# Kernel tuning notes

Hardware: AMD Instinct MI355X
Metric: run time of the kernel (lower is better)

The kernel has to match this reference:

```python
import jax, jax.numpy as jnp
import numpy as np
from jax import lax

B, NC, H, W = 8, 128, 64, 64
INP = 2 * NC            # 256 input_ch
UP = INP * 4            # 1024 upscaled_ch (r1=4)
MD = UP // 8            # 128 mamba_dim (r2=8)
IC = UP // 2            # 512 ghost init_channels (ratio=2)
DIN = 2 * MD            # 256 d_inner (expand=2)
DST = 1                 # d_state
DCONV = 4               # d_conv
DTR = 8                 # dt_rank = ceil(MD/16)
EPS = 1e-5

def _n(k, shape, fan):
    return jax.random.normal(k, shape, jnp.float32) / np.sqrt(fan)

def setup_inputs() -> dict:
    ks = jax.random.split(jax.random.key(0), 16)
    d = {}
    d['FT1'] = jax.random.normal(ks[0], (B, NC, H, W), jnp.float32)
    d['FT2'] = jax.random.normal(ks[1], (B, NC, H, W), jnp.float32)
    # GhostModule(inp=256, oup=1024): 1x1 primary + 3x3 depthwise cheap op
    d['g_primary_w'] = _n(ks[2], (IC, INP, 1, 1), INP)
    d['g_bn1_g'] = jnp.ones((IC,)); d['g_bn1_b'] = jnp.zeros((IC,))
    d['g_bn1_m'] = jnp.zeros((IC,)); d['g_bn1_v'] = jnp.ones((IC,))
    d['g_cheap_w'] = _n(ks[3], (IC, 1, 3, 3), 9)
    d['g_bn2_g'] = jnp.ones((IC,)); d['g_bn2_b'] = jnp.zeros((IC,))
    d['g_bn2_m'] = jnp.zeros((IC,)); d['g_bn2_v'] = jnp.ones((IC,))
    # SELayer(channel=1024, reduction=16), Linear bias=False
    d['se_w1'] = _n(ks[4], (UP // 16, UP), UP)
    d['se_w2'] = _n(ks[5], (UP, UP // 16), UP // 16)
    # 1x1 conv 1024->128 + BN
    d['proj_w'] = _n(ks[6], (MD, UP, 1, 1), UP)
    d['bn3_g'] = jnp.ones((MD,)); d['bn3_b'] = jnp.zeros((MD,))
    d['bn3_m'] = jnp.zeros((MD,)); d['bn3_v'] = jnp.ones((MD,))
    # Mamba(d_model=128, d_state=1, d_conv=4, expand=2)
    d['in_proj_w'] = _n(ks[7], (2 * DIN, MD), MD)
    d['conv1d_w'] = _n(ks[8], (DIN, 1, DCONV), DCONV)
    d['conv1d_b'] = jnp.zeros((DIN,))
    d['x_proj_w'] = _n(ks[9], (DTR + 2 * DST, DIN), DIN)
    d['dt_proj_w'] = _n(ks[10], (DIN, DTR), DTR)
    d['dt_proj_b'] = jnp.log(jnp.expm1(jnp.full((DIN,), 0.01)))  # softplus^-1(0.01)
    d['A_log'] = jnp.zeros((DIN, DST))  # A = -exp(0) = -1 (d_state=1 init)
    d['Dp'] = jnp.ones((DIN,))
    d['out_proj_w'] = _n(ks[11], (MD, DIN), DIN)
    # GatedResidual linear_pi: Linear(2*MD, MD) with bias
    d['pi_w'] = _n(ks[12], (MD, 2 * MD), 2 * MD)
    d['pi_b'] = jnp.zeros((MD,))
    # final 1x1 conv 128->128, no bias
    d['final_w'] = _n(ks[13], (NC, MD, 1, 1), MD)
    return d

def _bn(x, g, b, m, v):
    return (x - m[:, None, None]) * (g[:, None, None] / jnp.sqrt(v[:, None, None] + EPS)) + b[:, None, None]

def _conv2d(x, w, groups=1, pad=0):
    return lax.conv_general_dilated(x, w, (1, 1), [(pad, pad), (pad, pad)],
        dimension_numbers=('NCHW', 'OIHW', 'NCHW'), feature_group_count=groups)

def _mamba(x, in_proj_w, conv1d_w, conv1d_b, x_proj_w, dt_proj_w, dt_proj_b, A_log, Dp, out_proj_w):
    # x: (N, L, MD)
    N, L, _ = x.shape
    xz = x @ in_proj_w.T                    # (N,L,2*DIN)
    xs, z = jnp.split(xz, 2, axis=-1)
    # causal depthwise conv1d (pytorch pads d_conv-1 both sides then truncates to L)
    xc = jnp.moveaxis(xs, 1, 2)             # (N,DIN,L)
    xc = lax.conv_general_dilated(xc, conv1d_w, (1,), [(DCONV - 1, 0)],
        dimension_numbers=('NCH', 'OIH', 'NCH'), feature_group_count=DIN) + conv1d_b[:, None]
    u = jax.nn.silu(jnp.moveaxis(xc, 1, 2))  # (N,L,DIN)
    dbl = u @ x_proj_w.T                     # (N,L,DTR+2*DST)
    dt, Bm, Cm = dbl[..., :DTR], dbl[..., DTR:DTR + DST], dbl[..., DTR + DST:]
    dt = jax.nn.softplus(dt @ dt_proj_w.T + dt_proj_b)  # (N,L,DIN)
    A = -jnp.exp(A_log)                      # (DIN,DST)

    def step(h, inp):
        u_, dt_, B_, C_ = inp                # (N,DIN),(N,DIN),(N,DST),(N,DST)
        h = h * jnp.exp(dt_[:, :, None] * A) + dt_[:, :, None] * B_[:, None, :] * u_[:, :, None]
        return h, jnp.sum(h * C_[:, None, :], axis=-1)

    h0 = jnp.zeros((N, DIN, DST), x.dtype)
    _, y_t = lax.scan(step, h0, (jnp.moveaxis(u, 0, 1), jnp.moveaxis(dt, 0, 1),
                                 jnp.moveaxis(Bm, 0, 1), jnp.moveaxis(Cm, 0, 1)))
    y = jnp.moveaxis(y_t, 0, 1) + u * Dp
    y = y * jax.nn.silu(z)
    return y @ out_proj_w.T                  # (N,L,MD)

def reference(FT1, FT2, g_primary_w, g_bn1_g, g_bn1_b, g_bn1_m, g_bn1_v,
              g_cheap_w, g_bn2_g, g_bn2_b, g_bn2_m, g_bn2_v, se_w1, se_w2,
              proj_w, bn3_g, bn3_b, bn3_m, bn3_v, in_proj_w, conv1d_w, conv1d_b,
              x_proj_w, dt_proj_w, dt_proj_b, A_log, Dp, out_proj_w,
              pi_w, pi_b, final_w):
    Fcat = jnp.concatenate([FT1, FT2], axis=1)                       # (B,256,H,W)
    # GhostModule
    x1 = jax.nn.relu(_bn(_conv2d(Fcat, g_primary_w), g_bn1_g, g_bn1_b, g_bn1_m, g_bn1_v))
    x2 = jax.nn.relu(_bn(_conv2d(x1, g_cheap_w, groups=IC, pad=1), g_bn2_g, g_bn2_b, g_bn2_m, g_bn2_v))
    g = jnp.concatenate([x1, x2], axis=1)[:, :UP]                    # (B,1024,H,W)
    # SELayer
    s = jnp.mean(g, axis=(2, 3))
    s = jax.nn.sigmoid(jax.nn.relu(s @ se_w1.T) @ se_w2.T)
    g = g * s[:, :, None, None]
    Fp = _bn(_conv2d(g, proj_w), bn3_g, bn3_b, bn3_m, bn3_v)         # (B,MD,H,W)
    # four-way scan
    X_lr = jnp.transpose(Fp, (0, 2, 3, 1)).reshape(B, H * W, MD)
    X_rl = jnp.transpose(Fp[:, :, :, ::-1], (0, 2, 3, 1)).reshape(B, H * W, MD)
    X_ud = jnp.transpose(Fp, (0, 3, 2, 1)).reshape(B, H * W, MD)
    X_du = jnp.transpose(Fp[:, :, ::-1, :], (0, 3, 2, 1)).reshape(B, H * W, MD)
    X4 = jnp.stack([X_lr, X_rl, X_ud, X_du]).reshape(4 * B, H * W, MD)
    # shared Mamba block over all 4 directions in one batched call
    Y4 = _mamba(X4, in_proj_w, conv1d_w, conv1d_b, x_proj_w, dt_proj_w, dt_proj_b, A_log, Dp, out_proj_w)
    # gated residual
    pi = jax.nn.sigmoid(jnp.concatenate([X4, Y4], axis=-1) @ pi_w.T + pi_b)
    Yg = Y4 * pi + X4 * (1.0 - pi)
    # four-way inverse scan (sum, then row-major reshape as in source)
    y_sum = jnp.sum(Yg.reshape(4, B, H * W, MD), axis=0)
    f_scan = jnp.transpose(y_sum.reshape(B, H, W, MD), (0, 3, 1, 2))
    return _conv2d(f_scan + Fp, final_w)                             # (B,NC,H,W)
```

## Files before the change

kernel.cpp:

```cpp
#include <hip/hip_runtime.h>
#include <hip/hip_bf16.h>

#define DEV static __device__ __forceinline__

#define PIX 4096
#define SEQL 4096
#define BEPS 1e-5f

DEV float b2f(unsigned short u){ unsigned int i=((unsigned int)u)<<16; float f; __builtin_memcpy(&f,&i,4); return f; }
DEV unsigned short f2b(float f){ __hip_bfloat16 h=__float2bfloat16(f); unsigned short s; __builtin_memcpy(&s,&h,2); return s; }
DEV short f2bs(float f){ return (short)f2b(f); }
DEV void unp2(unsigned int w, float&a, float&b){ unsigned int lo=w<<16, hi=w&0xffff0000u; __builtin_memcpy(&a,&lo,4); __builtin_memcpy(&b,&hi,4); }
DEV unsigned int pk2(float a,float b){ return (unsigned int)f2b(a)|((unsigned int)f2b(b)<<16); }
DEV float sigm(float x){ return 1.f/(1.f+__expf(-x)); }
DEV float silu_(float x){ return x*sigm(x); }
DEV float softplus_(float x){ return (x>20.f)?x:log1pf(__expf(x)); }

using short8 = __attribute__((ext_vector_type(8))) short;
using f32x4  = __attribute__((ext_vector_type(4))) float;
#define MFMA16 __builtin_amdgcn_mfma_f32_16x16x32_bf16


#define MF_PRE() \
  const int tid=threadIdx.x; \
  const int lane=tid&63, wid=tid>>6; \
  const int wm=wid&1, wn=wid>>1; \
  const int fr=lane&15, fg=lane>>4; \
  const int srow=tid>>2, sch=tid&3; \
  const int tk=tid&63, tmb=(tid>>6)*16;

#define STAGE_A_TOK_BF(PTR) { \
  const unsigned short* ap_=(PTR); \
  uint4 q0_=*(const uint4*)ap_, q1_=*(const uint4*)(ap_+8); \
  int base_=srow*72+((sch^(srow&3))*16); \
  *(uint4*)&sA[base_]=q0_; *(uint4*)&sA[base_+8]=q1_; }

#define STAGE_A_SUM_BF(P1,P2) { \
  const unsigned short* p1_=(P1); const unsigned short* p2_=(P2); \
  unsigned short h1[16],h2[16]; \
  *(uint4*)&h1[0]=*(const uint4*)p1_; *(uint4*)&h1[8]=*(const uint4*)(p1_+8); \
  *(uint4*)&h2[0]=*(const uint4*)p2_; *(uint4*)&h2[8]=*(const uint4*)(p2_+8); \
  union { short h[16]; uint4 q[2]; } tmpa; \
  _Pragma("unroll") for(int j=0;j<16;++j) tmpa.h[j]=f2bs(b2f(h1[j])+b2f(h2[j])); \
  int base_=srow*72+((sch^(srow&3))*16); \
  *(uint4*)&sA[base_]=tmpa.q[0]; *(uint4*)&sA[base_+8]=tmpa.q[1]; }

#define STAGE_A_TR_F32(EXPR16) { \
  float tv[16]; \
  _Pragma("unroll") for(int j=0;j<16;++j) tv[j]=(EXPR16); \
  _Pragma("unroll") for(int j=0;j<16;++j){ int m_=tmb+j; \
    sA[m_*72+(((tk>>4)^(m_&3))<<4)+(tk&15)]=f2bs(tv[j]); } }

#define STAGE_A_TR_BF16(PTR) { \
  const unsigned short* ap_=(PTR); \
  unsigned short hv[16]; \
  *(uint4*)&hv[0]=*(const uint4*)ap_; *(uint4*)&hv[8]=*(const uint4*)(ap_+8); \
  _Pragma("unroll") for(int j=0;j<16;++j){ int m_=tmb+j; \
    sA[m_*72+(((tk>>4)^(m_&3))<<4)+(tk&15)]=(short)hv[j]; } }

#define STAGE_W_BF(PTR,LDK) { \
  const unsigned short* wp_=(PTR)+(size_t)(n0+srow)*(LDK)+k0+sch*16; \
  uint4 q0_=*(const uint4*)wp_, q1_=*(const uint4*)(wp_+8); \
  int sw_=((sch^(srow&3))*16); \
  *(uint4*)&sW[srow*72+sw_]=q0_; *(uint4*)&sW[srow*72+sw_+8]=q1_; }

#define MF_STEP() \
  _Pragma("unroll") \
  for(int kk=0;kk<64;kk+=32){ \
    short8 af[2],bfv[2]; const int kq_=kk+fg*8; \
    _Pragma("unroll") for(int i=0;i<2;++i){ int ml=wm*32+i*16+fr; \
      af[i]=*(const short8*)&sA[ml*72+(((kq_>>4)^(ml&3))<<4)+(kq_&15)]; } \
    _Pragma("unroll") for(int jn=0;jn<2;++jn){ int nl=wn*32+jn*16+fr; \
      bfv[jn]=*(const short8*)&sW[nl*72+(((kq_>>4)^(nl&3))<<4)+(kq_&15)]; } \
    _Pragma("unroll") for(int i=0;i<2;++i) \
      _Pragma("unroll") for(int jn=0;jn<2;++jn) \
        acc[i][jn]=MFMA16(af[i],bfv[jn],acc[i][jn],0,0,0); }

__global__ __launch_bounds__(256) void kWb(const float* __restrict__ g,const float* __restrict__ ip,
  const float* __restrict__ op,const float* __restrict__ pw,const float* __restrict__ f,
  unsigned short* __restrict__ gb,unsigned short* __restrict__ ib,unsigned short* __restrict__ ob,
  unsigned short* __restrict__ pb,unsigned short* __restrict__ fb)
{
  int x=blockIdx.x*256+threadIdx.x;
  if(x<131072) gb[x]=f2b(g[x]);
  if(x<65536)  ib[x]=f2b(ip[x]);
  if(x<32768){ ob[x]=f2b(op[x]); pb[x]=f2b(pw[x]); }
  if(x<16384)  fb[x]=f2b(f[x]);
}

__global__ __launch_bounds__(256) void kWc(const float* __restrict__ dtw,const float* __restrict__ xpw,
  unsigned short* __restrict__ Wcb)
{
  int c=blockIdx.x, k=threadIdx.x;
  float a=0.f;
  #pragma unroll
  for(int i=0;i<8;++i) a+=dtw[c*8+i]*xpw[i*256+k];
  Wcb[c*256+k]=f2b(a);
}

__global__ __launch_bounds__(256) void kWse(const float* __restrict__ prw,const float* __restrict__ sse,
  unsigned short* __restrict__ Wsb)
{
  int idx=blockIdx.x*256+threadIdx.x;
  int b=idx>>17, r=idx&131071, oc=r>>10, c=r&1023;
  Wsb[idx]=f2b(prw[(size_t)oc*1024+c]*sse[b*1024+c]);
}

__global__ __launch_bounds__(256) void k1m(const float* __restrict__ FT1,const float* __restrict__ FT2,
  const unsigned short* __restrict__ Wpb,const float* __restrict__ gg,const float* __restrict__ gb,
  const float* __restrict__ gm,const float* __restrict__ gv,unsigned short* __restrict__ x1)
{
  MF_PRE();
  __shared__ __align__(16) short sA[64*72];
  __shared__ __align__(16) short sW[64*72];
  const int m0=blockIdx.x*64, n0=blockIdx.y*64, b=blockIdx.z;
  f32x4 acc[2][2]={};
  for(int k0=0;k0<256;k0+=64){
    { int c=k0+tk;
      const float* s_=(c<128)? FT1+((size_t)b*128+c)*PIX : FT2+((size_t)b*128+c-128)*PIX;
      const float* ap=s_+m0+tmb;
      STAGE_A_TR_F32(ap[j]); }
    STAGE_W_BF(Wpb,256);
    __syncthreads();
    MF_STEP();
    __syncthreads();
  }
  #pragma unroll
  for(int jn=0;jn<2;++jn){ int oc=n0+wn*32+jn*16+fr;
    float ks=gg[oc]*rsqrtf(gv[oc]+BEPS), kb=gb[oc]-gm[oc]*ks;
    #pragma unroll
    for(int i=0;i<2;++i){ int mb=m0+wm*32+i*16+fg*4;
      float v0=fmaxf(acc[i][jn][0]*ks+kb,0.f), v1=fmaxf(acc[i][jn][1]*ks+kb,0.f);
      float v2=fmaxf(acc[i][jn][2]*ks+kb,0.f), v3=fmaxf(acc[i][jn][3]*ks+kb,0.f);
      uint2 pk; pk.x=pk2(v0,v1); pk.y=pk2(v2,v3);
      *(uint2*)&x1[((size_t)b*512+oc)*PIX+mb]=pk; } }
}

__global__ __launch_bounds__(256) void k2(const unsigned short* __restrict__ x1,const float* __restrict__ cw,
  const float* __restrict__ gg,const float* __restrict__ gb,const float* __restrict__ gm,
  const float* __restrict__ gv,unsigned short* __restrict__ x2)
{
  int gid=blockIdx.x*256+threadIdx.x;
  int wq=gid&15, h=(gid>>4)&63, bc=gid>>10;
  int c=bc&511;
  const unsigned short* src=x1+(size_t)bc*PIX;
  float wv[9];
  #pragma unroll
  for(int i=0;i<9;++i) wv[i]=cw[c*9+i];
  float ks=gg[c]*rsqrtf(gv[c]+BEPS), kb=gb[c]-gm[c]*ks;
  int wb=wq*4;
  float o[4]={};
  #pragma unroll
  for(int dh=0;dh<3;++dh){ int hh=h+dh-1; if(hh<0||hh>63) continue;
    const unsigned short* row=src+hh*64;
    float rv[6];
    #pragma unroll
    for(int j=0;j<6;++j){ int wc=wb-1+j; rv[j]=(wc>=0&&wc<64)?b2f(row[wc]):0.f; }
    #pragma unroll
    for(int dw=0;dw<3;++dw){ float wgt=wv[dh*3+dw];
      #pragma unroll
      for(int i=0;i<4;++i) o[i]+=rv[i+dw]*wgt; } }
  float v0=fmaxf(o[0]*ks+kb,0.f), v1=fmaxf(o[1]*ks+kb,0.f);
  float v2=fmaxf(o[2]*ks+kb,0.f), v3=fmaxf(o[3]*ks+kb,0.f);
  uint2 pk; pk.x=pk2(v0,v1); pk.y=pk2(v2,v3);
  *(uint2*)&x2[(size_t)bc*PIX+h*64+wb]=pk;
}

__global__ __launch_bounds__(256) void k3(const unsigned short* __restrict__ x1,
  const unsigned short* __restrict__ x2,float* __restrict__ sr)
{
  int bc=blockIdx.x; int cg=bc&1023, b=bc>>10;
  const unsigned short* src=(cg<512)? x1+((size_t)b*512+cg)*PIX : x2+((size_t)b*512+cg-512)*PIX;
  float s=0;
  for(int i=threadIdx.x;i<512;i+=256){
    uint4 v=((const uint4*)src)[i];
    float a0,a1; unp2(v.x,a0,a1); s+=a0+a1;
    unp2(v.y,a0,a1); s+=a0+a1;
    unp2(v.z,a0,a1); s+=a0+a1;
    unp2(v.w,a0,a1); s+=a0+a1;
  }
  #pragma unroll
  for(int off=32;off;off>>=1) s+=__shfl_down(s,off);
  __shared__ float red[4];
  if((threadIdx.x&63)==0) red[threadIdx.x>>6]=s;
  __syncthreads();
  if(threadIdx.x==0) sr[bc]=(red[0]+red[1]+red[2]+red[3])*(1.f/4096.f);
}

__global__ __launch_bounds__(256) void k4(const float* __restrict__ sr,const float* __restrict__ w1,
  const float* __restrict__ w2,float* __restrict__ sOut)
{
  int b=blockIdx.x;
  __shared__ float ls[1024];
  __shared__ float pm[4][64];
  __shared__ float mid[64];
  for(int i=threadIdx.x;i<1024;i+=256) ls[i]=sr[b*1024+i];
  __syncthreads();
  int k=threadIdx.x&63, part=threadIdx.x>>6;
  float p=0;
  for(int c=part*256;c<part*256+256;++c) p+=ls[c]*w1[k*1024+c];
  pm[part][k]=p;
  __syncthreads();
  if(threadIdx.x<64) mid[threadIdx.x]=fmaxf(pm[0][threadIdx.x]+pm[1][threadIdx.x]+pm[2][threadIdx.x]+pm[3][threadIdx.x],0.f);
  __syncthreads();
  for(int j=threadIdx.x;j<1024;j+=256){
    float a=0;
    for(int kk=0;kk<64;++kk) a+=mid[kk]*w2[j*64+kk];
    sOut[b*1024+j]=sigm(a);
  }
}

__global__ __launch_bounds__(256) void k5m(const unsigned short* __restrict__ x1,
  const unsigned short* __restrict__ x2,const unsigned short* __restrict__ Wsb,
  const float* __restrict__ g3,const float* __restrict__ b3,const float* __restrict__ m3,
  const float* __restrict__ v3,unsigned short* __restrict__ Fp,unsigned short* __restrict__ FpT)
{
  MF_PRE();
  __shared__ __align__(16) short sA[64*72];
  __shared__ __align__(16) short sW[64*72];
  const int m0=blockIdx.x*64, n0=blockIdx.y*64, b=blockIdx.z;
  const unsigned short* Wb=Wsb+(size_t)b*131072;
  f32x4 acc[2][2]={};
  for(int k0=0;k0<1024;k0+=64){
    { int c=k0+tk;
      const unsigned short* s_=(c<512)? x1+((size_t)b*512+c)*PIX : x2+((size_t)b*512+c-512)*PIX;
      STAGE_A_TR_BF16(s_+m0+tmb); }
    STAGE_W_BF(Wb,1024);
    __syncthreads();
    MF_STEP();
    __syncthreads();
  }
  #pragma unroll
  for(int jn=0;jn<2;++jn){ int oc=n0+wn*32+jn*16+fr;
    float ks=g3[oc]*rsqrtf(v3[oc]+BEPS), kb=b3[oc]-m3[oc]*ks;
    #pragma unroll
    for(int i=0;i<2;++i){ int mb=m0+wm*32+i*16+fg*4;
      #pragma unroll
      for(int p=0;p<4;++p){ int pp=mb+p; unsigned short val=f2b(acc[i][jn][p]*ks+kb);
        Fp[((size_t)b*PIX+pp)*128+oc]=val;
        int q=((pp&63)<<6)|(pp>>6);
        FpT[((size_t)b*PIX+q)*128+oc]=val; } } }
}

__global__ __launch_bounds__(256) void k6am(const unsigned short* __restrict__ Fp,
  const unsigned short* __restrict__ FpT,const unsigned short* __restrict__ Winb,
  unsigned short* __restrict__ xsT,unsigned short* __restrict__ zT)
{
  MF_PRE();
  __shared__ __align__(16) short sA[64*72];
  __shared__ __align__(16) short sW[64*72];
  const int m0=blockIdx.x*64, n0=blockIdx.y*64, n=blockIdx.z;
  const int d=n>>3, b=n&7;
  const unsigned short* src=((d<2)?Fp:FpT)+(size_t)b*PIX*128;
  const int rev=(d&1)?63:0;
  f32x4 acc[2][2]={};
  for(int k0=0;k0<128;k0+=64){
    { int t=m0+srow; int tm=(t&~63)|((t&63)^rev);
      STAGE_A_TOK_BF(src+(size_t)tm*128+k0+sch*16); }
    STAGE_W_BF(Winb,128);
    __syncthreads();
    MF_STEP();
    __syncthreads();
  }
  #pragma unroll
  for(int jn=0;jn<2;++jn){ int r=n0+wn*32+jn*16+fr;
    unsigned short* dst; int row; bool dosilu;
    if(r<256){ dst=xsT; row=r; dosilu=false; } else { dst=zT; row=r-256; dosilu=true; }
    #pragma unroll
    for(int i=0;i<2;++i){ int mb=m0+wm*32+i*16+fg*4;
      #pragma unroll
      for(int p=0;p<4;++p){ float v=acc[i][jn][p]; if(dosilu) v=silu_(v);
        dst[((size_t)n*SEQL+mb+p)*256+row]=f2b(v); } } }
}

__global__ __launch_bounds__(256) void k6b(const unsigned short* __restrict__ xsT,
  const float* __restrict__ cw,const float* __restrict__ cb,unsigned short* __restrict__ uT)
{
  int gid=blockIdx.x*256+threadIdx.x;
  int cb8=gid&31, tb=(gid>>5)&511, n=gid>>14;
  int c0=cb8*8, t0=tb*8;
  const unsigned short* base=xsT+(size_t)n*SEQL*256+c0;
  float w0[8],w1[8],w2[8],w3[8],bb[8];
  #pragma unroll
  for(int j=0;j<8;++j){ float4 wv=*(const float4*)&cw[(c0+j)*4];
    w0[j]=wv.x; w1[j]=wv.y; w2[j]=wv.z; w3[j]=wv.w; bb[j]=cb[c0+j]; }
  float ra[8],rb[8],rc[8],rd[8];
  #pragma unroll
  for(int j=0;j<8;++j){ ra[j]=0.f; rb[j]=0.f; rc[j]=0.f; }
  if(t0>=3){
    uint4 v;
    v=*(const uint4*)(base+(size_t)(t0-3)*256); unp2(v.x,ra[0],ra[1]);unp2(v.y,ra[2],ra[3]);unp2(v.z,ra[4],ra[5]);unp2(v.w,ra[6],ra[7]);
    v=*(const uint4*)(base+(size_t)(t0-2)*256); unp2(v.x,rb[0],rb[1]);unp2(v.y,rb[2],rb[3]);unp2(v.z,rb[4],rb[5]);unp2(v.w,rb[6],rb[7]);
    v=*(const uint4*)(base+(size_t)(t0-1)*256); unp2(v.x,rc[0],rc[1]);unp2(v.y,rc[2],rc[3]);unp2(v.z,rc[4],rc[5]);unp2(v.w,rc[6],rc[7]);
  }
  unsigned short* ob=uT+(size_t)n*SEQL*256+c0;
  for(int j=0;j<8;++j){
    uint4 v=*(const uint4*)(base+(size_t)(t0+j)*256);
    unp2(v.x,rd[0],rd[1]);unp2(v.y,rd[2],rd[3]);unp2(v.z,rd[4],rd[5]);unp2(v.w,rd[6],rd[7]);
    float o[8];
    #pragma unroll
    for(int q=0;q<8;++q){
      o[q]=silu_(ra[q]*w0[q]+rb[q]*w1[q]+rc[q]*w2[q]+rd[q]*w3[q]+bb[q]);
      ra[q]=rb[q]; rb[q]=rc[q]; rc[q]=rd[q];
    }
    uint4 ov; ov.x=pk2(o[0],o[1]); ov.y=pk2(o[2],o[3]); ov.z=pk2(o[4],o[5]); ov.w=pk2(o[6],o[7]);
    *(uint4*)(ob+(size_t)(t0+j)*256)=ov;
  }
}

__global__ __launch_bounds__(256) void k6cm(const unsigned short* __restrict__ uT,
  const unsigned short* __restrict__ Wcb,const float* __restrict__ dtb,
  unsigned short* __restrict__ dtT)
{
  MF_PRE();
  __shared__ __align__(16) short sA[64*72];
  __shared__ __align__(16) short sW[64*72];
  const int m0=blockIdx.x*64, n0=blockIdx.y*64, n=blockIdx.z;
  const unsigned short* ubase=uT+(size_t)n*SEQL*256;
  f32x4 acc[2][2]={};
  for(int k0=0;k0<256;k0+=64){
    STAGE_A_TOK_BF(ubase+(size_t)(m0+srow)*256+k0+sch*16);
    STAGE_W_BF(Wcb,256);
    __syncthreads();
    MF_STEP();
    __syncthreads();
  }
  #pragma unroll
  for(int jn=0;jn<2;++jn){ int oc=n0+wn*32+jn*16+fr;
    float bias=dtb[oc];
    #pragma unroll
    for(int i=0;i<2;++i){ int mb=m0+wm*32+i*16+fg*4;
      #pragma unroll
      for(int p=0;p<4;++p)
        dtT[((size_t)n*SEQL+mb+p)*256+oc]=f2b(softplus_(acc[i][jn][p]+bias)); } }
}

__global__ __launch_bounds__(256) void k6bc(const unsigned short* __restrict__ uT,
  const float* __restrict__ xpw,float* __restrict__ Bc,float* __restrict__ Cc)
{
  int inst=blockIdx.x*4+(threadIdx.x>>6);
  int ln=threadIdx.x&63;
  int n=inst>>12, t=inst&4095;
  const unsigned short* up=uT+((size_t)n*SEQL+t)*256+ln*4;
  uint2 uu=*(const uint2*)up;
  float u0,u1,u2,u3; unp2(uu.x,u0,u1); unp2(uu.y,u2,u3);
  float4 w8=*(const float4*)&xpw[8*256+ln*4];
  float4 w9=*(const float4*)&xpw[9*256+ln*4];
  float sb=u0*w8.x+u1*w8.y+u2*w8.z+u3*w8.w;
  float sc=u0*w9.x+u1*w9.y+u2*w9.z+u3*w9.w;
  #pragma unroll
  for(int off=32;off;off>>=1){ sb+=__shfl_xor(sb,off); sc+=__shfl_xor(sc,off); }
  if(ln==0){ Bc[(size_t)n*SEQL+t]=sb; Cc[(size_t)n*SEQL+t]=sc; }
}

__global__ __launch_bounds__(256) void k7p1(const unsigned short* __restrict__ uT,
  const unsigned short* __restrict__ dtT,const float* __restrict__ Bc,
  const float* __restrict__ A_log,float* __restrict__ Pq)
{
  int g=blockIdx.x*256+threadIdx.x;
  int cq=g&63, ch=(g>>6)&31, n=g>>11;
  int c0=cq*4;
  float A0=-__expf(A_log[c0]),A1=-__expf(A_log[c0+1]),A2=-__expf(A_log[c0+2]),A3=-__expf(A_log[c0+3]);
  size_t tbase=((size_t)n*SEQL+ch*128)*256+c0;
  const float* bp=Bc+(size_t)n*SEQL+ch*128;
  float P0=1,P1=1,P2=1,P3=1,q0=0,q1=0,q2=0,q3=0;
  for(int t=0;t<128;++t){
    uint2 uu=*(const uint2*)&uT[tbase+(size_t)t*256];
    uint2 dd=*(const uint2*)&dtT[tbase+(size_t)t*256];
    float u0,u1,u2,u3,d0,d1,d2,d3;
    unp2(uu.x,u0,u1); unp2(uu.y,u2,u3);
    unp2(dd.x,d0,d1); unp2(dd.y,d2,d3);
    float bv=bp[t];
    float e0=__expf(d0*A0),e1=__expf(d1*A1),e2=__expf(d2*A2),e3=__expf(d3*A3);
    q0=q0*e0+d0*bv*u0; q1=q1*e1+d1*bv*u1; q2=q2*e2+d2*bv*u2; q3=q3*e3+d3*bv*u3;
    P0*=e0; P1*=e1; P2*=e2; P3*=e3;
  }
  size_t o=(((size_t)n*256+c0)*32+ch)*2;
  Pq[o]=P0; Pq[o+1]=q0; Pq[o+64]=P1; Pq[o+65]=q1;
  Pq[o+128]=P2; Pq[o+129]=q2; Pq[o+192]=P3; Pq[o+193]=q3;
}

__global__ __launch_bounds__(256) void k7mid(const float* __restrict__ Pq,float* __restrict__ h0)
{
  int nc=blockIdx.x*256+threadIdx.x;
  float h=0.f;
  for(int ch=0;ch<32;++ch){
    h0[(size_t)nc*32+ch]=h;
    h=h*Pq[((size_t)nc*32+ch)*2]+Pq[((size_t)nc*32+ch)*2+1];
  }
}

__global__ __launch_bounds__(256) void k7p2(unsigned short* __restrict__ uT,
  const unsigned short* __restrict__ dtT,const unsigned short* __restrict__ zT,
  const float* __restrict__ Bc,const float* __restrict__ Cc,
  const float* __restrict__ A_log,const float* __restrict__ Dp,
  const float* __restrict__ h0)
{
  int g=blockIdx.x*256+threadIdx.x;
  int cq=g&63, ch=(g>>6)&31, n=g>>11;
  int c0=cq*4;
  float A0=-__expf(A_log[c0]),A1=-__expf(A_log[c0+1]),A2=-__expf(A_log[c0+2]),A3=-__expf(A_log[c0+3]);
  float D0=Dp[c0],D1=Dp[c0+1],D2=Dp[c0+2],D3=Dp[c0+3];
  size_t tbase=((size_t)n*SEQL+ch*128)*256+c0;
  const float* bp=Bc+(size_t)n*SEQL+ch*128;
  const float* cp=Cc+(size_t)n*SEQL+ch*128;
  size_t hb=((size_t)n*256+c0)*32+ch;
  float h0v=h0[hb],h1v=h0[hb+32],h2v=h0[hb+64],h3v=h0[hb+96];
  for(int t=0;t<128;++t){
    uint2 uu=*(const uint2*)&uT[tbase+(size_t)t*256];
    uint2 dd=*(const uint2*)&dtT[tbase+(size_t)t*256];
    uint2 zz=*(const uint2*)&zT[tbase+(size_t)t*256];
    float u0,u1,u2,u3,d0,d1,d2,d3,z0,z1,z2,z3;
    unp2(uu.x,u0,u1); unp2(uu.y,u2,u3);
    unp2(dd.x,d0,d1); unp2(dd.y,d2,d3);
    unp2(zz.x,z0,z1); unp2(zz.y,z2,z3);
    float bv=bp[t], cv=cp[t];
    float e0=__expf(d0*A0),e1=__expf(d1*A1),e2=__expf(d2*A2),e3=__expf(d3*A3);
    h0v=h0v*e0+d0*bv*u0; h1v=h1v*e1+d1*bv*u1; h2v=h2v*e2+d2*bv*u2; h3v=h3v*e3+d3*bv*u3;
    float y0=(h0v*cv+u0*D0)*z0, y1=(h1v*cv+u1*D1)*z1;
    float y2=(h2v*cv+u2*D2)*z2, y3=(h3v*cv+u3*D3)*z3;
    uint2 oo; oo.x=pk2(y0,y1); oo.y=pk2(y2,y3);
    *(uint2*)&uT[tbase+(size_t)t*256]=oo;
  }
}

__global__ __launch_bounds__(256) void k8am(const unsigned short* __restrict__ yT,
  const unsigned short* __restrict__ Woutb,unsigned short* __restrict__ Y4)
{
  MF_PRE();
  __shared__ __align__(16) short sA[64*72];
  __shared__ __align__(16) short sW[64*72];
  const int m0=blockIdx.x*64, n0=blockIdx.y*64, n=blockIdx.z;
  const unsigned short* ybase=yT+(size_t)n*SEQL*256;
  f32x4 acc[2][2]={};
  for(int k0=0;k0<256;k0+=64){
    STAGE_A_TOK_BF(ybase+(size_t)(m0+srow)*256+k0+sch*16);
    STAGE_W_BF(Woutb,256);
    __syncthreads();
    MF_STEP();
    __syncthreads();
  }
  #pragma unroll
  for(int jn=0;jn<2;++jn){ int oc=n0+wn*32+jn*16+fr;
    #pragma unroll
    for(int i=0;i<2;++i){ int mb=m0+wm*32+i*16+fg*4;
      #pragma unroll
      for(int p=0;p<4;++p)
        Y4[((size_t)n*SEQL+mb+p)*128+oc]=f2b(acc[i][jn][p]); } }
}

__global__ __launch_bounds__(256) void k8bm(const unsigned short* __restrict__ Fp,
  const unsigned short* __restrict__ FpT,const unsigned short* __restrict__ Y4,
  const unsigned short* __restrict__ piwb,const float* __restrict__ pib,
  unsigned short* __restrict__ ysum)
{
  MF_PRE();
  __shared__ __align__(16) short sA[64*72];
  __shared__ __align__(16) short sW[64*72];
  const int m0=blockIdx.x*64, n0=blockIdx.y*64, b=blockIdx.z;
  f32x4 gs[2][2]={};
  for(int d=0;d<4;++d){
    const int n=d*8+b;
    const unsigned short* src=((d<2)?Fp:FpT)+(size_t)b*PIX*128;
    const int rev=(d&1)?63:0;
    f32x4 acc[2][2]={};
    for(int k0=0;k0<256;k0+=64){
      if(k0<128){
        int t=m0+srow; int tm=(t&~63)|((t&63)^rev);
        STAGE_A_TOK_BF(src+(size_t)tm*128+k0+sch*16);
      } else {
        STAGE_A_TOK_BF(Y4+((size_t)n*SEQL+m0+srow)*128+(k0-128)+sch*16);
      }
      STAGE_W_BF(piwb,256);
      __syncthreads();
      MF_STEP();
      __syncthreads();
    }
    #pragma unroll
    for(int i=0;i<2;++i){
      #pragma unroll
      for(int jn=0;jn<2;++jn){
        int oc=n0+wn*32+jn*16+fr;
        int mb=m0+wm*32+i*16+fg*4;
        float pb=pib[oc];
        #pragma unroll
        for(int p=0;p<4;++p){
          int t=mb+p; int tm=(t&~63)|((t&63)^rev);
          float pi=sigm(acc[i][jn][p]+pb);
          float x4=b2f(src[(size_t)tm*128+oc]);
          float y4=b2f(Y4[((size_t)n*SEQL+t)*128+oc]);
          gs[i][jn][p]+=y4*pi+x4*(1.f-pi);
        }
      }
    }
  }
  #pragma unroll
  for(int i=0;i<2;++i)
    #pragma unroll
    for(int jn=0;jn<2;++jn){
      int oc=n0+wn*32+jn*16+fr;
      int mb=m0+wm*32+i*16+fg*4;
      #pragma unroll
      for(int p=0;p<4;++p)
        ysum[((size_t)b*PIX+mb+p)*128+oc]=f2b(gs[i][jn][p]);
    }
}

__global__ __launch_bounds__(256) void k9m(const unsigned short* __restrict__ ysum,
  const unsigned short* __restrict__ Fp,const unsigned short* __restrict__ fwb,
  float* __restrict__ out)
{
  MF_PRE();
  __shared__ __align__(16) short sA[64*72];
  __shared__ __align__(16) short sW[64*72];
  const int m0=blockIdx.x*64, n0=blockIdx.y*64, b=blockIdx.z;
  f32x4 acc[2][2]={};
  for(int k0=0;k0<128;k0+=64){
    { size_t off=((size_t)b*PIX+m0+srow)*128+k0+sch*16;
      STAGE_A_SUM_BF(ysum+off,Fp+off); }
    STAGE_W_BF(fwb,128);
    __syncthreads();
    MF_STEP();
    __syncthreads();
  }
  #pragma unroll
  for(int jn=0;jn<2;++jn){ int oc=n0+wn*32+jn*16+fr;
    #pragma unroll
    for(int i=0;i<2;++i){ int mb=m0+wm*32+i*16+fg*4;
      *(float4*)&out[((size_t)b*128+oc)*PIX+mb]=
        make_float4(acc[i][jn][0],acc[i][jn][1],acc[i][jn][2],acc[i][jn][3]); } }
}

extern "C" void kernel_launch(void* const* d_in,const int* in_sizes,int n_in,
  void* d_out,int out_size,void* d_ws,size_t ws_size,hipStream_t stream)
{
  (void)in_sizes; (void)n_in; (void)out_size; (void)ws_size;
  const float* FT1=(const float*)d_in[0];
  const float* FT2=(const float*)d_in[1];
  const float* gpw=(const float*)d_in[2];
  const float* g1g=(const float*)d_in[3];
  const float* g1b=(const float*)d_in[4];
  const float* g1m=(const float*)d_in[5];
  const float* g1v=(const float*)d_in[6];
  const float* gcw=(const float*)d_in[7];
  const float* g2g=(const float*)d_in[8];
  const float* g2b=(const float*)d_in[9];
  const float* g2m=(const float*)d_in[10];
  const float* g2v=(const float*)d_in[11];
  const float* sw1=(const float*)d_in[12];
  const float* sw2=(const float*)d_in[13];
  const float* prw=(const float*)d_in[14];
  const float* b3g=(const float*)d_in[15];
  const float* b3b=(const float*)d_in[16];
  const float* b3m=(const float*)d_in[17];
  const float* b3v=(const float*)d_in[18];
  const float* ipw=(const float*)d_in[19];
  const float* c1w=(const float*)d_in[20];
  const float* c1b=(const float*)d_in[21];
  const float* xpw=(const float*)d_in[22];
  const float* dtw=(const float*)d_in[23];
  const float* dtb=(const float*)d_in[24];
  const float* Alog=(const float*)d_in[25];
  const float* Dp=(const float*)d_in[26];
  const float* opw=(const float*)d_in[27];
  const float* piw=(const float*)d_in[28];
  const float* pib=(const float*)d_in[29];
  const float* fw=(const float*)d_in[30];

  char* w=(char*)d_ws;
  const size_t MB=1ull<<20;
  unsigned short* x1b =(unsigned short*)(w);
  unsigned short* x2b =(unsigned short*)(w+32*MB);
  unsigned short* uT  =(unsigned short*)(w);
  unsigned short* xsT =(unsigned short*)(w+64*MB);
  unsigned short* dtT =(unsigned short*)(w+64*MB);
  unsigned short* Y4  =(unsigned short*)(w+64*MB);
  unsigned short* zT  =(unsigned short*)(w+128*MB);
  unsigned short* Fpb =(unsigned short*)(w+192*MB);
  unsigned short* FpTb=(unsigned short*)(w+200*MB);
  unsigned short* ysb =(unsigned short*)(w+208*MB);
  float* Bc =(float*)(w+216*MB);
  float* Cc =(float*)(w+216*MB+512*1024);
  float* sr =(float*)(w+217*MB);
  float* sse=(float*)(w+217*MB+32*1024);
  float* Pq =(float*)(w+218*MB);
  float* h0 =(float*)(w+220*MB);
  unsigned short* Wcb =(unsigned short*)(w+221*MB);
  unsigned short* gpwb=(unsigned short*)(w+222*MB);
  unsigned short* ipwb=(unsigned short*)(w+223*MB);
  unsigned short* opwb=(unsigned short*)(w+224*MB);
  unsigned short* piwb=(unsigned short*)(w+224*MB+64*1024);
  unsigned short* fwb =(unsigned short*)(w+224*MB+128*1024);
  unsigned short* Wsb =(unsigned short*)(w+225*MB);

  kWb<<<512,256,0,stream>>>(gpw,ipw,opw,piw,fw,gpwb,ipwb,opwb,piwb,fwb);
  kWc<<<256,256,0,stream>>>(dtw,xpw,Wcb);
  k1m<<<dim3(64,8,8),256,0,stream>>>(FT1,FT2,gpwb,g1g,g1b,g1m,g1v,x1b);
  k2<<<16384,256,0,stream>>>(x1b,gcw,g2g,g2b,g2m,g2v,x2b);
  k3<<<8192,256,0,stream>>>(x1b,x2b,sr);
  k4<<<8,256,0,stream>>>(sr,sw1,sw2,sse);
  kWse<<<4096,256,0,stream>>>(prw,sse,Wsb);
  k5m<<<dim3(64,2,8),256,0,stream>>>(x1b,x2b,Wsb,b3g,b3b,b3m,b3v,Fpb,FpTb);
  k6am<<<dim3(64,8,32),256,0,stream>>>(Fpb,FpTb,ipwb,xsT,zT);
  k6b<<<2048,256,0,stream>>>(xsT,c1w,c1b,uT);
  k6cm<<<dim3(64,4,32),256,0,stream>>>(uT,Wcb,dtb,dtT);
  k6bc<<<32768,256,0,stream>>>(uT,xpw,Bc,Cc);
  k7p1<<<256,256,0,stream>>>(uT,dtT,Bc,Alog,Pq);
  k7mid<<<32,256,0,stream>>>(Pq,h0);
  k7p2<<<256,256,0,stream>>>(uT,dtT,zT,Bc,Cc,Alog,Dp,h0);
  k8am<<<dim3(64,2,32),256,0,stream>>>(uT,opwb,Y4);
  k8bm<<<dim3(64,2,8),256,0,stream>>>(Fpb,FpTb,Y4,piwb,pib,ysb);
  k9m<<<dim3(64,2,8),256,0,stream>>>(ysb,Fpb,fwb,(float*)d_out);
}
```

Measured before the change: 637.3 us.

## Enlarge MFMA GEMM tiles and add register prefetch of next K tile

Several 1x1-conv and projection GEMM kernels (k1m, k5m, k6am, k6cm, k8am, k8bm) move from 64x64 tiles to 64x128 or 128x128 tiles, so each wave computes a 2x4 or 4x4 block of 16x16 MFMA outputs and the A and weight tiles are loaded fewer times. The token-major kernels also load the next K-slice into registers while the current slice is being computed. The aim is to raise arithmetic intensity and hide global load latency. In exchange, register and LDS use per block go up and the grids shrink (k8bm to 256 blocks, k5m to 512), which may lower occupancy and leave compute units underused.

Result: slower. 845.7 us (+32.7%).

```diff
diff --git a/kernel.cpp b/kernel.cpp
--- a/kernel.cpp
+++ b/kernel.cpp
@@ -21,19 +21,67 @@
 #define MFMA16 __builtin_amdgcn_mfma_f32_16x16x32_bf16
 
 
+#define VA_PRE() \
+  const int tid=threadIdx.x, lane=tid&63, wid=tid>>6; \
+  const int wm=wid&1, wn=wid>>1, fr=lane&15, fg=lane>>4; \
+  const int crow=tid>>2, sch=tid&3;
+
+#define VA_LOAD(R, P0, P1) { \
+  R[0]=*(const uint4*)(P0); R[1]=*(const uint4*)((P0)+8); \
+  R[2]=*(const uint4*)(P1); R[3]=*(const uint4*)((P1)+8); }
+
+#define VA_WRITE(DST, R) { \
+  int b1_=crow*72+((sch^(crow&3))*16); \
+  *(uint4*)&DST[b1_]=R[0]; *(uint4*)&DST[b1_+8]=R[1]; \
+  *(uint4*)&DST[b1_+64*72]=R[2]; *(uint4*)&DST[b1_+64*72+8]=R[3]; }
+
+#define VA_STEP() \
+  _Pragma("unroll") \
+  for(int kk=0;kk<64;kk+=32){ \
+    short8 af[4],bf[4]; const int kq_=kk+fg*8; \
+    _Pragma("unroll") for(int i=0;i<4;++i){ int ml=wm*64+i*16+fr; \
+      af[i]=*(const short8*)&sA[ml*72+(((kq_>>4)^(ml&3))<<4)+(kq_&15)]; } \
+    _Pragma("unroll") for(int j=0;j<4;++j){ int nl=wn*64+j*16+fr; \
+      bf[j]=*(const short8*)&sW[nl*72+(((kq_>>4)^(nl&3))<<4)+(kq_&15)]; } \
+    _Pragma("unroll") for(int i=0;i<4;++i) \
+      _Pragma("unroll") for(int j=0;j<4;++j) \
+        acc[i][j]=MFMA16(af[i],bf[j],acc[i][j],0,0,0); }
+
+#define VB_PRE() \
+  const int tid=threadIdx.x, lane=tid&63, wid=tid>>6; \
+  const int wm=wid&1, wn=wid>>1, fr=lane&15, fg=lane>>4; \
+  const int crow=tid>>2, sch=tid&3; \
+  const int tk=tid&63, tmb=(tid>>6)*16;
+
+#define VB_STEP() \
+  _Pragma("unroll") \
+  for(int kk=0;kk<64;kk+=32){ \
+    short8 af[2],bf[4]; const int kq_=kk+fg*8; \
+    _Pragma("unroll") for(int i=0;i<2;++i){ int ml=wm*32+i*16+fr; \
+      af[i]=*(const short8*)&sA[ml*72+(((kq_>>4)^(ml&3))<<4)+(kq_&15)]; } \
+    _Pragma("unroll") for(int j=0;j<4;++j){ int nl=wn*64+j*16+fr; \
+      bf[j]=*(const short8*)&sW[nl*72+(((kq_>>4)^(nl&3))<<4)+(kq_&15)]; } \
+    _Pragma("unroll") for(int i=0;i<2;++i) \
+      _Pragma("unroll") for(int j=0;j<4;++j) \
+        acc[i][j]=MFMA16(af[i],bf[j],acc[i][j],0,0,0); }
+
+#define STAGE_A_TR_F32(EXPR16) { \
+  float tv[16]; \
+  _Pragma("unroll") for(int j=0;j<16;++j) tv[j]=(EXPR16); \
+  _Pragma("unroll") for(int j=0;j<16;++j){ int m_=tmb+j; \
+    sA[m_*72+(((tk>>4)^(m_&3))<<4)+(tk&15)]=f2bs(tv[j]); } }
+
+#define STAGE_A_TR_BF16(PTR) { \
+  const unsigned short* ap_=(PTR); \
+  unsigned short hv[16]; \
+  *(uint4*)&hv[0]=*(const uint4*)ap_; *(uint4*)&hv[8]=*(const uint4*)(ap_+8); \
+  _Pragma("unroll") for(int j=0;j<16;++j){ int m_=tmb+j; \
+    sA[m_*72+(((tk>>4)^(m_&3))<<4)+(tk&15)]=(short)hv[j]; } }
+
 #define MF_PRE() \
-  const int tid=threadIdx.x; \
-  const int lane=tid&63, wid=tid>>6; \
-  const int wm=wid&1, wn=wid>>1; \
-  const int fr=lane&15, fg=lane>>4; \
-  const int srow=tid>>2, sch=tid&3; \
-  const int tk=tid&63, tmb=(tid>>6)*16;
-
-#define STAGE_A_TOK_BF(PTR) { \
-  const unsigned short* ap_=(PTR); \
-  uint4 q0_=*(const uint4*)ap_, q1_=*(const uint4*)(ap_+8); \
-  int base_=srow*72+((sch^(srow&3))*16); \
-  *(uint4*)&sA[base_]=q0_; *(uint4*)&sA[base_+8]=q1_; }
+  const int tid=threadIdx.x, lane=tid&63, wid=tid>>6; \
+  const int wm=wid&1, wn=wid>>1, fr=lane&15, fg=lane>>4; \
+  const int srow=tid>>2, sch=tid&3;
 
 #define STAGE_A_SUM_BF(P1,P2) { \
   const unsigned short* p1_=(P1); const unsigned short* p2_=(P2); \
@@ -44,19 +92,6 @@
   _Pragma("unroll") for(int j=0;j<16;++j) tmpa.h[j]=f2bs(b2f(h1[j])+b2f(h2[j])); \
   int base_=srow*72+((sch^(srow&3))*16); \
   *(uint4*)&sA[base_]=tmpa.q[0]; *(uint4*)&sA[base_+8]=tmpa.q[1]; }
-
-#define STAGE_A_TR_F32(EXPR16) { \
-  float tv[16]; \
-  _Pragma("unroll") for(int j=0;j<16;++j) tv[j]=(EXPR16); \
-  _Pragma("unroll") for(int j=0;j<16;++j){ int m_=tmb+j; \
-    sA[m_*72+(((tk>>4)^(m_&3))<<4)+(tk&15)]=f2bs(tv[j]); } }
-
-#define STAGE_A_TR_BF16(PTR) { \
-  const unsigned short* ap_=(PTR); \
-  unsigned short hv[16]; \
-  *(uint4*)&hv[0]=*(const uint4*)ap_; *(uint4*)&hv[8]=*(const uint4*)(ap_+8); \
-  _Pragma("unroll") for(int j=0;j<16;++j){ int m_=tmb+j; \
-    sA[m_*72+(((tk>>4)^(m_&3))<<4)+(tk&15)]=(short)hv[j]; } }
 
 #define STAGE_W_BF(PTR,LDK) { \
   const unsigned short* wp_=(PTR)+(size_t)(n0+srow)*(LDK)+k0+sch*16; \
@@ -110,23 +145,25 @@
   const unsigned short* __restrict__ Wpb,const float* __restrict__ gg,const float* __restrict__ gb,
   const float* __restrict__ gm,const float* __restrict__ gv,unsigned short* __restrict__ x1)
 {
-  MF_PRE();
+  VB_PRE();
   __shared__ __align__(16) short sA[64*72];
-  __shared__ __align__(16) short sW[64*72];
-  const int m0=blockIdx.x*64, n0=blockIdx.y*64, b=blockIdx.z;
-  f32x4 acc[2][2]={};
+  __shared__ __align__(16) short sW[128*72];
+  const int m0=blockIdx.x*64, n0=blockIdx.y*128, b=blockIdx.z;
+  f32x4 acc[2][4]={};
   for(int k0=0;k0<256;k0+=64){
     { int c=k0+tk;
       const float* s_=(c<128)? FT1+((size_t)b*128+c)*PIX : FT2+((size_t)b*128+c-128)*PIX;
       const float* ap=s_+m0+tmb;
       STAGE_A_TR_F32(ap[j]); }
-    STAGE_W_BF(Wpb,256);
-    __syncthreads();
-    MF_STEP();
-    __syncthreads();
-  }
-  #pragma unroll
-  for(int jn=0;jn<2;++jn){ int oc=n0+wn*32+jn*16+fr;
+    { uint4 pw[4];
+      VA_LOAD(pw, Wpb+(size_t)(n0+crow)*256+k0+sch*16, Wpb+(size_t)(n0+crow+64)*256+k0+sch*16);
+      VA_WRITE(sW,pw); }
+    __syncthreads();
+    VB_STEP();
+    __syncthreads();
+  }
+  #pragma unroll
+  for(int jn=0;jn<4;++jn){ int oc=n0+wn*64+jn*16+fr;
     float ks=gg[oc]*rsqrtf(gv[oc]+BEPS), kb=gb[oc]-gm[oc]*ks;
     #pragma unroll
     for(int i=0;i<2;++i){ int mb=m0+wm*32+i*16+fg*4;
@@ -215,23 +252,25 @@
   const float* __restrict__ g3,const float* __restrict__ b3,const float* __restrict__ m3,
   const float* __restrict__ v3,unsigned short* __restrict__ Fp,unsigned short* __restrict__ FpT)
 {
-  MF_PRE();
+  VB_PRE();
   __shared__ __align__(16) short sA[64*72];
-  __shared__ __align__(16) short sW[64*72];
-  const int m0=blockIdx.x*64, n0=blockIdx.y*64, b=blockIdx.z;
+  __shared__ __align__(16) short sW[128*72];
+  const int m0=blockIdx.x*64, n0=0, b=blockIdx.z;
   const unsigned short* Wb=Wsb+(size_t)b*131072;
-  f32x4 acc[2][2]={};
+  f32x4 acc[2][4]={};
   for(int k0=0;k0<1024;k0+=64){
     { int c=k0+tk;
       const unsigned short* s_=(c<512)? x1+((size_t)b*512+c)*PIX : x2+((size_t)b*512+c-512)*PIX;
       STAGE_A_TR_BF16(s_+m0+tmb); }
-    STAGE_W_BF(Wb,1024);
-    __syncthreads();
-    MF_STEP();
-    __syncthreads();
-  }
-  #pragma unroll
-  for(int jn=0;jn<2;++jn){ int oc=n0+wn*32+jn*16+fr;
+    { uint4 pw[4];
+      VA_LOAD(pw, Wb+(size_t)(n0+crow)*1024+k0+sch*16, Wb+(size_t)(n0+crow+64)*1024+k0+sch*16);
+      VA_WRITE(sW,pw); }
+    __syncthreads();
+    VB_STEP();
+    __syncthreads();
+  }
+  #pragma unroll
+  for(int jn=0;jn<4;++jn){ int oc=n0+wn*64+jn*16+fr;
     float ks=g3[oc]*rsqrtf(v3[oc]+BEPS), kb=b3[oc]-m3[oc]*ks;
     #pragma unroll
     for(int i=0;i<2;++i){ int mb=m0+wm*32+i*16+fg*4;
@@ -246,28 +285,36 @@
   const unsigned short* __restrict__ FpT,const unsigned short* __restrict__ Winb,
   unsigned short* __restrict__ xsT,unsigned short* __restrict__ zT)
 {
-  MF_PRE();
-  __shared__ __align__(16) short sA[64*72];
-  __shared__ __align__(16) short sW[64*72];
-  const int m0=blockIdx.x*64, n0=blockIdx.y*64, n=blockIdx.z;
+  VA_PRE();
+  __shared__ __align__(16) short sA[128*72];
+  __shared__ __align__(16) short sW[128*72];
+  const int m0=blockIdx.x*128, n0=blockIdx.y*128, n=blockIdx.z;
   const int d=n>>3, b=n&7;
   const unsigned short* src=((d<2)?Fp:FpT)+(size_t)b*PIX*128;
   const int rev=(d&1)?63:0;
-  f32x4 acc[2][2]={};
+  const int t1=m0+crow, t2=m0+crow+64;
+  const size_t ro1=(size_t)((t1&~63)|((t1&63)^rev))*128;
+  const size_t ro2=(size_t)((t2&~63)|((t2&63)^rev))*128;
+  f32x4 acc[4][4]={};
+  uint4 pa[4],pw[4];
+  VA_LOAD(pa, src+ro1+sch*16, src+ro2+sch*16);
+  VA_LOAD(pw, Winb+(size_t)(n0+crow)*128+sch*16, Winb+(size_t)(n0+crow+64)*128+sch*16);
   for(int k0=0;k0<128;k0+=64){
-    { int t=m0+srow; int tm=(t&~63)|((t&63)^rev);
-      STAGE_A_TOK_BF(src+(size_t)tm*128+k0+sch*16); }
-    STAGE_W_BF(Winb,128);
-    __syncthreads();
-    MF_STEP();
-    __syncthreads();
-  }
-  #pragma unroll
-  for(int jn=0;jn<2;++jn){ int r=n0+wn*32+jn*16+fr;
+    VA_WRITE(sA,pa); VA_WRITE(sW,pw);
+    __syncthreads();
+    if(k0==0){
+      VA_LOAD(pa, src+ro1+64+sch*16, src+ro2+64+sch*16);
+      VA_LOAD(pw, Winb+(size_t)(n0+crow)*128+64+sch*16, Winb+(size_t)(n0+crow+64)*128+64+sch*16);
+    }
+    VA_STEP();
+    __syncthreads();
+  }
+  #pragma unroll
+  for(int jn=0;jn<4;++jn){ int r=n0+wn*64+jn*16+fr;
     unsigned short* dst; int row; bool dosilu;
     if(r<256){ dst=xsT; row=r; dosilu=false; } else { dst=zT; row=r-256; dosilu=true; }
     #pragma unroll
-    for(int i=0;i<2;++i){ int mb=m0+wm*32+i*16+fg*4;
+    for(int i=0;i<4;++i){ int mb=m0+wm*64+i*16+fg*4;
       #pragma unroll
       for(int p=0;p<4;++p){ float v=acc[i][jn][p]; if(dosilu) v=silu_(v);
         dst[((size_t)n*SEQL+mb+p)*256+row]=f2b(v); } } }
@@ -312,24 +359,31 @@
   const unsigned short* __restrict__ Wcb,const float* __restrict__ dtb,
   unsigned short* __restrict__ dtT)
 {
-  MF_PRE();
-  __shared__ __align__(16) short sA[64*72];
-  __shared__ __align__(16) short sW[64*72];
-  const int m0=blockIdx.x*64, n0=blockIdx.y*64, n=blockIdx.z;
-  const unsigned short* ubase=uT+(size_t)n*SEQL*256;
-  f32x4 acc[2][2]={};
+  VA_PRE();
+  __shared__ __align__(16) short sA[128*72];
+  __shared__ __align__(16) short sW[128*72];
+  const int m0=blockIdx.x*128, n0=blockIdx.y*128, n=blockIdx.z;
+  const unsigned short* u1=uT+(size_t)n*SEQL*256+(size_t)(m0+crow)*256;
+  const unsigned short* u2=u1+(size_t)64*256;
+  f32x4 acc[4][4]={};
+  uint4 pa[4],pw[4];
+  VA_LOAD(pa, u1+sch*16, u2+sch*16);
+  VA_LOAD(pw, Wcb+(size_t)(n0+crow)*256+sch*16, Wcb+(size_t)(n0+crow+64)*256+sch*16);
   for(int k0=0;k0<256;k0+=64){
-    STAGE_A_TOK_BF(ubase+(size_t)(m0+srow)*256+k0+sch*16);
-    STAGE_W_BF(Wcb,256);
-    __syncthreads();
-    MF_STEP();
-    __syncthreads();
-  }
-  #pragma unroll
-  for(int jn=0;jn<2;++jn){ int oc=n0+wn*32+jn*16+fr;
+    VA_WRITE(sA,pa); VA_WRITE(sW,pw);
+    __syncthreads();
+    if(k0<192){
+      VA_LOAD(pa, u1+k0+64+sch*16, u2+k0+64+sch*16);
+      VA_LOAD(pw, Wcb+(size_t)(n0+crow)*256+k0+64+sch*16, Wcb+(size_t)(n0+crow+64)*256+k0+64+sch*16);
+    }
+    VA_STEP();
+    __syncthreads();
+  }
+  #pragma unroll
+  for(int jn=0;jn<4;++jn){ int oc=n0+wn*64+jn*16+fr;
     float bias=dtb[oc];
     #pragma unroll
-    for(int i=0;i<2;++i){ int mb=m0+wm*32+i*16+fg*4;
+    for(int i=0;i<4;++i){ int mb=m0+wm*64+i*16+fg*4;
       #pragma unroll
       for(int p=0;p<4;++p)
         dtT[((size_t)n*SEQL+mb+p)*256+oc]=f2b(softplus_(acc[i][jn][p]+bias)); } }
@@ -427,26 +481,41 @@
 __global__ __launch_bounds__(256) void k8am(const unsigned short* __restrict__ yT,
   const unsigned short* __restrict__ Woutb,unsigned short* __restrict__ Y4)
 {
-  MF_PRE();
-  __shared__ __align__(16) short sA[64*72];
-  __shared__ __align__(16) short sW[64*72];
-  const int m0=blockIdx.x*64, n0=blockIdx.y*64, n=blockIdx.z;
-  const unsigned short* ybase=yT+(size_t)n*SEQL*256;
-  f32x4 acc[2][2]={};
+  VA_PRE();
+  __shared__ __align__(16) short sA[128*72];
+  __shared__ __align__(16) short sW[128*72];
+  const int m0=blockIdx.x*128, n0=0, n=blockIdx.z;
+  const unsigned short* u1=yT+(size_t)n*SEQL*256+(size_t)(m0+crow)*256;
+  const unsigned short* u2=u1+(size_t)64*256;
+  f32x4 acc[4][4]={};
+  uint4 pa[4],pw[4];
+  VA_LOAD(pa, u1+sch*16, u2+sch*16);
+  VA_LOAD(pw, Woutb+(size_t)(n0+crow)*256+sch*16, Woutb+(size_t)(n0+crow+64)*256+sch*16);
   for(int k0=0;k0<256;k0+=64){
-    STAGE_A_TOK_BF(ybase+(size_t)(m0+srow)*256+k0+sch*16);
-    STAGE_W_BF(Woutb,256);
-    __syncthreads();
-    MF_STEP();
-    __syncthreads();
-  }
-  #pragma unroll
-  for(int jn=0;jn<2;++jn){ int oc=n0+wn*32+jn*16+fr;
-    #pragma unroll
-    for(int i=0;i<2;++i){ int mb=m0+wm*32+i*16+fg*4;
+    VA_WRITE(sA,pa); VA_WRITE(sW,pw);
+    __syncthreads();
+    if(k0<192){
+      VA_LOAD(pa, u1+k0+64+sch*16, u2+k0+64+sch*16);
+      VA_LOAD(pw, Woutb+(size_t)(n0+crow)*256+k0+64+sch*16, Woutb+(size_t)(n0+crow+64)*256+k0+64+sch*16);
+    }
+    VA_STEP();
+    __syncthreads();
+  }
+  #pragma unroll
+  for(int jn=0;jn<4;++jn){ int oc=n0+wn*64+jn*16+fr;
+    #pragma unroll
+    for(int i=0;i<4;++i){ int mb=m0+wm*64+i*16+fg*4;
       #pragma unroll
       for(int p=0;p<4;++p)
         Y4[((size_t)n*SEQL+mb+p)*128+oc]=f2b(acc[i][jn][p]); } }
+}
+
+DEV const unsigned short* k8b_aptr(const unsigned short* src,const unsigned short* Y4n,
+  int m0,int r,int rev,int k0p,int sch)
+{
+  if(k0p<128){ int t=m0+r; int tm=(t&~63)|((t&63)^rev);
+    return src+(size_t)tm*128+k0p+sch*16; }
+  return Y4n+(size_t)(m0+r)*128+(k0p-128)+sch*16;
 }
 
 __global__ __launch_bounds__(256) void k8bm(const unsigned short* __restrict__ Fp,
@@ -454,52 +523,54 @@
   const unsigned short* __restrict__ piwb,const float* __restrict__ pib,
   unsigned short* __restrict__ ysum)
 {
-  MF_PRE();
-  __shared__ __align__(16) short sA[64*72];
-  __shared__ __align__(16) short sW[64*72];
-  const int m0=blockIdx.x*64, n0=blockIdx.y*64, b=blockIdx.z;
-  f32x4 gs[2][2]={};
+  VA_PRE();
+  __shared__ __align__(16) short sA[128*72];
+  __shared__ __align__(16) short sW[128*72];
+  const int m0=blockIdx.x*128, n0=0, b=blockIdx.z;
+  f32x4 gs[4][4]={};
   for(int d=0;d<4;++d){
     const int n=d*8+b;
     const unsigned short* src=((d<2)?Fp:FpT)+(size_t)b*PIX*128;
+    const unsigned short* Y4n=Y4+(size_t)n*SEQL*128;
     const int rev=(d&1)?63:0;
-    f32x4 acc[2][2]={};
+    f32x4 acc[4][4]={};
+    uint4 pa[4],pw[4];
+    VA_LOAD(pa, k8b_aptr(src,Y4n,m0,crow,rev,0,sch), k8b_aptr(src,Y4n,m0,crow+64,rev,0,sch));
+    VA_LOAD(pw, piwb+(size_t)(n0+crow)*256+sch*16, piwb+(size_t)(n0+crow+64)*256+sch*16);
     for(int k0=0;k0<256;k0+=64){
-      if(k0<128){
-        int t=m0+srow; int tm=(t&~63)|((t&63)^rev);
-        STAGE_A_TOK_BF(src+(size_t)tm*128+k0+sch*16);
-      } else {
-        STAGE_A_TOK_BF(Y4+((size_t)n*SEQL+m0+srow)*128+(k0-128)+sch*16);
+      VA_WRITE(sA,pa); VA_WRITE(sW,pw);
+      __syncthreads();
+      if(k0<192){
+        VA_LOAD(pa, k8b_aptr(src,Y4n,m0,crow,rev,k0+64,sch), k8b_aptr(src,Y4n,m0,crow+64,rev,k0+64,sch));
+        VA_LOAD(pw, piwb+(size_t)(n0+crow)*256+k0+64+sch*16, piwb+(size_t)(n0+crow+64)*256+k0+64+sch*16);
       }
-      STAGE_W_BF(piwb,256);
-      __syncthreads();
-      MF_STEP();
+      VA_STEP();
       __syncthreads();
     }
     #pragma unroll
-    for(int i=0;i<2;++i){
+    for(int i=0;i<4;++i){
       #pragma unroll
-      for(int jn=0;jn<2;++jn){
-        int oc=n0+wn*32+jn*16+fr;
-        int mb=m0+wm*32+i*16+fg*4;
+      for(int jn=0;jn<4;++jn){
+        int oc=n0+wn*64+jn*16+fr;
+        int mb=m0+wm*64+i*16+fg*4;
         float pb=pib[oc];
         #pragma unroll
         for(int p=0;p<4;++p){
           int t=mb+p; int tm=(t&~63)|((t&63)^rev);
           float pi=sigm(acc[i][jn][p]+pb);
           float x4=b2f(src[(size_t)tm*128+oc]);
-          float y4=b2f(Y4[((size_t)n*SEQL+t)*128+oc]);
+          float y4=b2f(Y4n[(size_t)t*128+oc]);
           gs[i][jn][p]+=y4*pi+x4*(1.f-pi);
         }
       }
     }
   }
   #pragma unroll
-  for(int i=0;i<2;++i)
-    #pragma unroll
-    for(int jn=0;jn<2;++jn){
-      int oc=n0+wn*32+jn*16+fr;
-      int mb=m0+wm*32+i*16+fg*4;
+  for(int i=0;i<4;++i)
+    #pragma unroll
+    for(int jn=0;jn<4;++jn){
+      int oc=n0+wn*64+jn*16+fr;
+      int mb=m0+wm*64+i*16+fg*4;
       #pragma unroll
       for(int p=0;p<4;++p)
         ysum[((size_t)b*PIX+mb+p)*128+oc]=f2b(gs[i][jn][p]);
@@ -595,20 +666,20 @@
 
   kWb<<<512,256,0,stream>>>(gpw,ipw,opw,piw,fw,gpwb,ipwb,opwb,piwb,fwb);
   kWc<<<256,256,0,stream>>>(dtw,xpw,Wcb);
-  k1m<<<dim3(64,8,8),256,0,stream>>>(FT1,FT2,gpwb,g1g,g1b,g1m,g1v,x1b);
+  k1m<<<dim3(64,4,8),256,0,stream>>>(FT1,FT2,gpwb,g1g,g1b,g1m,g1v,x1b);
   k2<<<16384,256,0,stream>>>(x1b,gcw,g2g,g2b,g2m,g2v,x2b);
   k3<<<8192,256,0,stream>>>(x1b,x2b,sr);
   k4<<<8,256,0,stream>>>(sr,sw1,sw2,sse);
   kWse<<<4096,256,0,stream>>>(prw,sse,Wsb);
-  k5m<<<dim3(64,2,8),256,0,stream>>>(x1b,x2b,Wsb,b3g,b3b,b3m,b3v,Fpb,FpTb);
-  k6am<<<dim3(64,8,32),256,0,stream>>>(Fpb,FpTb,ipwb,xsT,zT);
+  k5m<<<dim3(64,1,8),256,0,stream>>>(x1b,x2b,Wsb,b3g,b3b,b3m,b3v,Fpb,FpTb);
+  k6am<<<dim3(32,4,32),256,0,stream>>>(Fpb,FpTb,ipwb,xsT,zT);
   k6b<<<2048,256,0,stream>>>(xsT,c1w,c1b,uT);
-  k6cm<<<dim3(64,4,32),256,0,stream>>>(uT,Wcb,dtb,dtT);
+  k6cm<<<dim3(32,2,32),256,0,stream>>>(uT,Wcb,dtb,dtT);
   k6bc<<<32768,256,0,stream>>>(uT,xpw,Bc,Cc);
   k7p1<<<256,256,0,stream>>>(uT,dtT,Bc,Alog,Pq);
   k7mid<<<32,256,0,stream>>>(Pq,h0);
   k7p2<<<256,256,0,stream>>>(uT,dtT,zT,Bc,Cc,Alog,Dp,h0);
-  k8am<<<dim3(64,2,32),256,0,stream>>>(uT,opwb,Y4);
-  k8bm<<<dim3(64,2,8),256,0,stream>>>(Fpb,FpTb,Y4,piwb,pib,ysb);
+  k8am<<<dim3(32,1,32),256,0,stream>>>(uT,opwb,Y4);
+  k8bm<<<dim3(32,1,8),256,0,stream>>>(Fpb,FpTb,Y4,piwb,pib,ysb);
   k9m<<<dim3(64,2,8),256,0,stream>>>(ysb,Fpb,fwb,(float*)d_out);
 }
```
